# Optimization experiments

Hardware: AMD Instinct MI355X
Metric: run time of the kernel (lower is better)

## Reference

```python
import jax, jax.numpy as jnp
import numpy as np

N, D = 131072, 128   # total nodes, feature size (input_size)
G, L = 512, 448      # num graphs, max padded segment length
EPS = 1e-5


def setup_inputs() -> dict:
    key = jax.random.key(0)
    ks = jax.random.split(key, 8)
    # ragged segment sizes summing exactly to N, each <= L
    rng = np.random.default_rng(0)
    counts = rng.integers(192, 321, size=G)
    diff = N - int(counts.sum())
    idx = rng.integers(0, G, size=abs(diff))
    np.add.at(counts, idx, 1 if diff > 0 else -1)
    assert int(counts.sum()) == N and int(counts.max()) <= L
    batch = jnp.asarray(np.repeat(np.arange(G), counts), dtype=jnp.int32)

    s = 1.0 / np.sqrt(D)
    x = jax.random.normal(ks[0], (N, D), jnp.float32)
    Wk = jax.random.normal(ks[1], (D, D), jnp.float32) * s
    Wq = jax.random.normal(ks[2], (D, D), jnp.float32) * s
    Wv = jax.random.normal(ks[3], (D, D), jnp.float32) * s
    bk = jnp.zeros((D,), jnp.float32)
    bq = jnp.zeros((D,), jnp.float32)
    bv = jnp.zeros((D,), jnp.float32)
    gamma = jnp.ones((D,), jnp.float32)
    beta = jnp.zeros((D,), jnp.float32)
    return {"x": x, "Wk": Wk, "bk": bk, "Wq": Wq, "bq": bq,
            "Wv": Wv, "bv": bv, "gamma": gamma, "beta": beta, "batch": batch}


def reference(x, Wk, bk, Wq, bq, Wv, bv, gamma, beta, batch):
    keys = x @ Wk.T + bk
    query = x @ Wq.T + bq
    values = x @ Wv.T + bv

    counts = jnp.bincount(batch, length=G)                 # [G]
    starts = jnp.cumsum(counts) - counts                   # segment offsets
    pos = jnp.arange(N, dtype=batch.dtype) - starts[batch]  # index within segment

    # scatter ragged nodes into padded [G, L, D] blocks (honors block-diagonal structure)
    kp = jnp.zeros((G, L, D), x.dtype).at[batch, pos].set(keys)
    qp = jnp.zeros((G, L, D), x.dtype).at[batch, pos].set(query)
    vp = jnp.zeros((G, L, D), x.dtype).at[batch, pos].set(values)
    valid = jnp.arange(L)[None, :] < counts[:, None]        # [G, L]

    # NOTE: original computes softmax(K @ Q^T / sqrt(dk)) @ V (keys as rows)
    scale = 1.0 / jnp.sqrt(jnp.asarray(D, x.dtype))
    scores = jnp.einsum('gld,gmd->glm', kp, qp) * scale     # [G, L, L]
    scores = jnp.where(valid[:, None, :], scores, jnp.asarray(-1e9, x.dtype))
    attn = jax.nn.softmax(scores, axis=-1)
    zp = jnp.einsum('glm,gmd->gld', attn, vp)               # [G, L, D]
    z = zp[batch, pos]                                      # back to ragged [N, D]

    h = x + z
    mu = jnp.mean(h, axis=-1, keepdims=True)
    var = jnp.var(h, axis=-1, keepdims=True)
    return (h - mu) / jnp.sqrt(var + EPS) * gamma + beta
```

## Files before the change

### kernel.cpp

```cpp
#include <hip/hip_runtime.h>
#include <hip/hip_bf16.h>

#define N_NODES 131072
#define DIM 128
#define NG 512

typedef __bf16 bf16;
typedef __attribute__((ext_vector_type(8))) __bf16 bf16x8;
typedef __attribute__((ext_vector_type(4))) float f32x4;

#define KSC 0.12753785006196978f

#define WS_STARTS 0
#define WS_WF     8192
#define WS_KB     131072
#define WS_QB     (131072 + 33554432)
#define WS_VTB    (131072 + 2*33554432)

__device__ __forceinline__ void gl_lds16(const void* g, void* l) {
    __builtin_amdgcn_global_load_lds(
        (const __attribute__((address_space(1))) unsigned int*)g,
        (__attribute__((address_space(3))) unsigned int*)l, 16, 0, 0);
}

__global__ void seg_starts_kernel(const int* __restrict__ batch, int* __restrict__ starts) {
    int g = threadIdx.x;
    int lo = 0, hi = N_NODES;
    while (lo < hi) { int mid = (lo + hi) >> 1; if (batch[mid] < g) lo = mid + 1; else hi = mid; }
    starts[g] = lo;
    if (g == 0) starts[NG] = N_NODES;
}

__global__ void wconv_kernel(const float* __restrict__ Wk, const float* __restrict__ Wq,
                             const float* __restrict__ Wv, bf16* __restrict__ Wf) {
    int f = blockIdx.x * 256 + threadIdx.x;
    int lane = f & 63, ks = (f >> 6) & 3, n0 = (f >> 8) & 7, mat = f >> 11;
    const float* src = (mat == 0) ? Wk : ((mat == 1) ? Wq : Wv);
    float sc = (mat == 0) ? KSC : 1.0f;
    int col = n0 * 16 + (lane & 15);
    int koff = ks * 32 + (lane >> 4) * 8;
    const float* p = src + col * DIM + koff;
    bf16* dst = Wf + (size_t)f * 8;
    #pragma unroll
    for (int j = 0; j < 8; j++) dst[j] = (bf16)(p[j] * sc);
}

__global__ __launch_bounds__(256) void qkv_kernel(
        const float* __restrict__ x, const bf16* __restrict__ Wf,
        const float* __restrict__ bk, const float* __restrict__ bq, const float* __restrict__ bv,
        bf16* __restrict__ Kb, bf16* __restrict__ Qb, bf16* __restrict__ Vtb) {
    __shared__ bf16 tile[128 * 136];
    const int tid = threadIdx.x;
    const int w = tid >> 6, lane = tid & 63, q = lane >> 4, i = lane & 15;
    const int r0 = blockIdx.x * 128;

    {
        #pragma unroll
        for (int it = 0; it < 16; it++) {
            int e = tid * 4 + it * 1024;
            int row = e >> 7, col = e & 127;
            float4 u = *(const float4*)(x + (size_t)(r0 + row) * DIM + col);
            bf16 b[4] = {(bf16)u.x, (bf16)u.y, (bf16)u.z, (bf16)u.w};
            *(ushort4*)&tile[row * 136 + col] = *(ushort4*)b;
        }
    }
    __syncthreads();

    bf16x8 af[2][4];
    #pragma unroll
    for (int rg = 0; rg < 2; rg++)
        #pragma unroll
        for (int ks = 0; ks < 4; ks++)
            af[rg][ks] = *(const bf16x8*)&tile[(w * 32 + rg * 16 + i) * 136 + ks * 32 + q * 8];
    __syncthreads();

    for (int mat = 0; mat < 3; mat++) {
        const float* bias = (mat == 0) ? bk : ((mat == 1) ? bq : bv);
        const float bscale = (mat == 0) ? KSC : 1.0f;
        for (int n0 = 0; n0 < 8; n0++) {
            int col = n0 * 16 + i;
            float bias_v = bias[col] * bscale;
            f32x4 acc0 = {0,0,0,0}, acc1 = {0,0,0,0};
            #pragma unroll
            for (int ks = 0; ks < 4; ks++) {
                bf16x8 bw = *(const bf16x8*)(Wf + ((size_t)((mat * 8 + n0) * 4 + ks) * 64 + lane) * 8);
                acc0 = __builtin_amdgcn_mfma_f32_16x16x32_bf16(af[0][ks], bw, acc0, 0, 0, 0);
                acc1 = __builtin_amdgcn_mfma_f32_16x16x32_bf16(af[1][ks], bw, acc1, 0, 0, 0);
            }
            #pragma unroll
            for (int rg = 0; rg < 2; rg++) {
                f32x4 a = rg ? acc1 : acc0;
                #pragma unroll
                for (int r = 0; r < 4; r++) {
                    int rowl = w * 32 + rg * 16 + q * 4 + r;
                    bf16 hv = (bf16)(a[r] + bias_v);
                    if (mat < 2) tile[rowl * 136 + col] = hv;
                    else         tile[col * 136 + rowl] = hv;
                }
            }
        }
        __syncthreads();
        {
            int row = tid >> 1, half = tid & 1;
            const uint4* src = (const uint4*)(tile + row * 136 + half * 64);
            uint4* dst;
            if (mat == 0)      dst = (uint4*)(Kb  + (size_t)(r0 + row) * DIM + half * 64);
            else if (mat == 1) dst = (uint4*)(Qb  + (size_t)(r0 + row) * DIM + half * 64);
            else               dst = (uint4*)(Vtb + (size_t)row * N_NODES + r0 + half * 64);
            #pragma unroll
            for (int j = 0; j < 8; j++) dst[j] = src[j];
        }
        __syncthreads();
    }
}

__global__ __launch_bounds__(256, 2) void attn_kernel(
        const float* __restrict__ x,
        const bf16* __restrict__ Kb, const bf16* __restrict__ Qb, const bf16* __restrict__ Vtb,
        const float* __restrict__ gamma, const float* __restrict__ beta,
        const int* __restrict__ starts, float* __restrict__ out) {
    __shared__ bf16 Qs[2][64 * 128];
    __shared__ bf16 Vts[2][128 * 64];
    __shared__ bf16 Ps[4][32 * 64];

    const int g = blockIdx.y;
    const int seg = starts[g];
    const int c = starts[g + 1] - seg;
    const int l0 = blockIdx.x * 128;
    if (l0 >= c) return;

    const int tid = threadIdx.x;
    const int w = tid >> 6, lane = tid & 63, q = lane >> 4, i = lane & 15;

    const int mstart = seg & ~7;
    const int nch = (seg - mstart + c + 63) >> 6;

    auto stage = [&](int buf, int mb) {
        const int rb = w * 16;
        #pragma unroll
        for (int p = 0; p < 4; p++) {
            int row = rb + p * 4 + (lane >> 4);
            int gr = mb + row; if (gr > N_NODES - 1) gr = N_NODES - 1;
            gl_lds16(Qb + (size_t)gr * DIM + (((lane & 15) ^ (row & 7)) << 3),
                     &Qs[buf][(rb + p * 4) * 128]);
        }
        const int db = w * 32;
        #pragma unroll
        for (int p = 0; p < 4; p++) {
            int d = db + p * 8 + (lane >> 3);
            int mo = mb + (((lane & 7) ^ (d & 7)) << 3);
            if (mo > N_NODES - 8) mo = N_NODES - 8;
            gl_lds16(Vtb + (size_t)d * N_NODES + mo,
                     &Vts[buf][(db + p * 8) * 64]);
        }
    };

    stage(0, mstart);

    bf16x8 afK[2][4];
    #pragma unroll
    for (int rg = 0; rg < 2; rg++) {
        int lrow = l0 + w * 32 + rg * 16 + i;
        if (lrow > c - 1) lrow = c - 1;
        const bf16* krow = Kb + (size_t)(seg + lrow) * DIM;
        #pragma unroll
        for (int ks = 0; ks < 4; ks++)
            afK[rg][ks] = *(const bf16x8*)(krow + ks * 32 + q * 8);
    }

    float li[2][4] = {{0,0,0,0},{0,0,0,0}};
    f32x4 Oc[2][8];
    #pragma unroll
    for (int rg = 0; rg < 2; rg++)
        #pragma unroll
        for (int t = 0; t < 8; t++) Oc[rg][t] = (f32x4){0,0,0,0};

    bf16* Pw = Ps[w];
    const int f7 = i & 7;
    const int mh = (i >> 3);

    for (int mc = 0; mc < nch; mc++) {
        const int cur = mc & 1;
        const int mbase = mstart + (mc << 6);
        __syncthreads();
        if (mc + 1 < nch) stage(cur ^ 1, mbase + 64);

        const bf16* QsB = Qs[cur];
        const bf16* VtB = Vts[cur];

        #pragma unroll
        for (int ti = 0; ti < 4; ti++) {
            f32x4 a0 = {0,0,0,0}, a1 = {0,0,0,0};
            #pragma unroll
            for (int ks = 0; ks < 4; ks++) {
                bf16x8 bq = *(const bf16x8*)&QsB[(ti * 16 + i) * 128 + (((ks * 4 + q) ^ f7) << 3)];
                a0 = __builtin_amdgcn_mfma_f32_16x16x32_bf16(afK[0][ks], bq, a0, 0, 0, 0);
                a1 = __builtin_amdgcn_mfma_f32_16x16x32_bf16(afK[1][ks], bq, a1, 0, 0, 0);
            }
            if (mc == 0 || mc == nch - 1) {
                int mg = mbase + ti * 16 + i;
                if (mg < seg || mg >= seg + c) {
                    a0 = (f32x4){-1.0e30f, -1.0e30f, -1.0e30f, -1.0e30f};
                    a1 = a0;
                }
            }
            int mhi = 2 * ti + mh;
            #pragma unroll
            for (int r = 0; r < 4; r++) {
                int lr = q * 4 + r;
                int sl = ((mhi ^ (lr & 7)) << 3) + f7;
                float p0 = exp2f(a0[r]); li[0][r] += p0;
                Pw[lr * 64 + sl] = (bf16)p0;
                float p1 = exp2f(a1[r]); li[1][r] += p1;
                Pw[(16 + lr) * 64 + sl] = (bf16)p1;
            }
        }

        bf16x8 afP[2][2];
        #pragma unroll
        for (int rg = 0; rg < 2; rg++)
            #pragma unroll
            for (int k2 = 0; k2 < 2; k2++)
                afP[rg][k2] = *(const bf16x8*)&Pw[(rg * 16 + i) * 64 + (((k2 * 4 + q) ^ f7) << 3)];

        #pragma unroll
        for (int dt = 0; dt < 8; dt++) {
            #pragma unroll
            for (int k2 = 0; k2 < 2; k2++) {
                bf16x8 bv = *(const bf16x8*)&VtB[(dt * 16 + i) * 64 + (((k2 * 4 + q) ^ f7) << 3)];
                Oc[0][dt] = __builtin_amdgcn_mfma_f32_16x16x32_bf16(afP[0][k2], bv, Oc[0][dt], 0, 0, 0);
                Oc[1][dt] = __builtin_amdgcn_mfma_f32_16x16x32_bf16(afP[1][k2], bv, Oc[1][dt], 0, 0, 0);
            }
        }
    }

    #pragma unroll
    for (int st = 1; st < 16; st <<= 1)
        #pragma unroll
        for (int rg = 0; rg < 2; rg++)
            #pragma unroll
            for (int r = 0; r < 4; r++)
                li[rg][r] += __shfl_xor(li[rg][r], st);

    float gv[8], bvv[8];
    #pragma unroll
    for (int t = 0; t < 8; t++) { gv[t] = gamma[t * 16 + i]; bvv[t] = beta[t * 16 + i]; }
    #pragma unroll
    for (int rg = 0; rg < 2; rg++)
        for (int r = 0; r < 4; r++) {
            int lg = l0 + w * 32 + rg * 16 + q * 4 + r;
            if (lg >= c) continue;
            size_t node = (size_t)(seg + lg);
            float inv = 1.0f / li[rg][r];
            const float* xr = x + node * DIM;
            float h[8], sum = 0.0f, ss = 0.0f;
            #pragma unroll
            for (int t = 0; t < 8; t++) {
                float hv = xr[t * 16 + i] + Oc[rg][t][r] * inv;
                h[t] = hv;
                sum += hv; ss += hv * hv;
            }
            #pragma unroll
            for (int st = 1; st < 16; st <<= 1) {
                sum += __shfl_xor(sum, st);
                ss  += __shfl_xor(ss, st);
            }
            float mu = sum * (1.0f / 128.0f);
            float var = ss * (1.0f / 128.0f) - mu * mu;
            float rstd = rsqrtf(var + 1e-5f);
            float* op = out + node * DIM;
            #pragma unroll
            for (int t = 0; t < 8; t++)
                op[t * 16 + i] = (h[t] - mu) * rstd * gv[t] + bvv[t];
        }
}

extern "C" void kernel_launch(void* const* d_in, const int* in_sizes, int n_in,
                              void* d_out, int out_size, void* d_ws, size_t ws_size,
                              hipStream_t stream) {
    (void)in_sizes; (void)n_in; (void)out_size; (void)ws_size;
    const float* x     = (const float*)d_in[0];
    const float* Wk    = (const float*)d_in[1];
    const float* bk    = (const float*)d_in[2];
    const float* Wq    = (const float*)d_in[3];
    const float* bq    = (const float*)d_in[4];
    const float* Wv    = (const float*)d_in[5];
    const float* bv    = (const float*)d_in[6];
    const float* gamma = (const float*)d_in[7];
    const float* beta  = (const float*)d_in[8];
    const int*   batch = (const int*)d_in[9];
    float* out = (float*)d_out;

    char* ws = (char*)d_ws;
    int*  starts = (int*)(ws + WS_STARTS);
    bf16* Wf  = (bf16*)(ws + WS_WF);
    bf16* Kb  = (bf16*)(ws + WS_KB);
    bf16* Qb  = (bf16*)(ws + WS_QB);
    bf16* Vtb = (bf16*)(ws + WS_VTB);

    seg_starts_kernel<<<1, 512, 0, stream>>>(batch, starts);
    wconv_kernel<<<24, 256, 0, stream>>>(Wk, Wq, Wv, Wf);
    qkv_kernel<<<1024, 256, 0, stream>>>(x, Wf, bk, bq, bv, Kb, Qb, Vtb);
    attn_kernel<<<dim3(4, NG), 256, 0, stream>>>(x, Kb, Qb, Vtb, gamma, beta, starts, out);
}
```

Measured before the change: 277.3 us.

## Triple-buffer attention chunks at 32 keys, reuse Q LDS for P, raise occupancy

The attention kernel now processes 32-key chunks with a 3-stage LDS ring buffer, using explicit vmcnt waits and raw barriers so loads run two chunks ahead. The separate P scratch buffer is removed and P is written into the consumed Q buffer, which cuts LDS use so launch bounds can rise to 3 blocks per CU. It also adds MFMA priority hints and swaps the grid so graph is on the x dimension. Smaller chunks mean more barriers per key, and the hand-written waitcnt logic relies on exact load counts per stage.

```diff
diff --git a/kernel.cpp b/kernel.cpp
--- a/kernel.cpp
+++ b/kernel.cpp
@@ -114,48 +114,44 @@
     }
 }
 
-__global__ __launch_bounds__(256, 2) void attn_kernel(
+__global__ __launch_bounds__(256, 3) void attn_kernel(
         const float* __restrict__ x,
         const bf16* __restrict__ Kb, const bf16* __restrict__ Qb, const bf16* __restrict__ Vtb,
         const float* __restrict__ gamma, const float* __restrict__ beta,
         const int* __restrict__ starts, float* __restrict__ out) {
-    __shared__ bf16 Qs[2][64 * 128];
-    __shared__ bf16 Vts[2][128 * 64];
-    __shared__ bf16 Ps[4][32 * 64];
-
-    const int g = blockIdx.y;
+    __shared__ bf16 Qs[3][32 * 128];
+    __shared__ bf16 Vts[3][128 * 32];
+
+    const int g = blockIdx.x;
     const int seg = starts[g];
     const int c = starts[g + 1] - seg;
-    const int l0 = blockIdx.x * 128;
+    const int l0 = blockIdx.y * 128;
     if (l0 >= c) return;
 
     const int tid = threadIdx.x;
     const int w = tid >> 6, lane = tid & 63, q = lane >> 4, i = lane & 15;
 
     const int mstart = seg & ~7;
-    const int nch = (seg - mstart + c + 63) >> 6;
+    const int nch = (seg - mstart + c + 31) >> 5;
 
     auto stage = [&](int buf, int mb) {
-        const int rb = w * 16;
-        #pragma unroll
-        for (int p = 0; p < 4; p++) {
-            int row = rb + p * 4 + (lane >> 4);
+        #pragma unroll
+        for (int p = 0; p < 2; p++) {
+            int row = w * 8 + p * 4 + (lane >> 4);
             int gr = mb + row; if (gr > N_NODES - 1) gr = N_NODES - 1;
             gl_lds16(Qb + (size_t)gr * DIM + (((lane & 15) ^ (row & 7)) << 3),
-                     &Qs[buf][(rb + p * 4) * 128]);
-        }
-        const int db = w * 32;
-        #pragma unroll
-        for (int p = 0; p < 4; p++) {
-            int d = db + p * 8 + (lane >> 3);
-            int mo = mb + (((lane & 7) ^ (d & 7)) << 3);
+                     &Qs[buf][(w * 8 + p * 4) * 128]);
+        }
+        #pragma unroll
+        for (int p = 0; p < 2; p++) {
+            int d = w * 32 + p * 16 + (lane >> 2);
+            int tvd = ((lane >> 2) ^ (lane >> 4)) & 3;
+            int mo = mb + (((lane & 3) ^ tvd) << 3);
             if (mo > N_NODES - 8) mo = N_NODES - 8;
             gl_lds16(Vtb + (size_t)d * N_NODES + mo,
-                     &Vts[buf][(db + p * 8) * 64]);
+                     &Vts[buf][(w * 32 + p * 16) * 32]);
         }
     };
-
-    stage(0, mstart);
 
     bf16x8 afK[2][4];
     #pragma unroll
@@ -168,6 +164,9 @@
             afK[rg][ks] = *(const bf16x8*)(krow + ks * 32 + q * 8);
     }
 
+    stage(0, mstart);
+    if (nch > 1) stage(1, mstart + 32);
+
     float li[2][4] = {{0,0,0,0},{0,0,0,0}};
     f32x4 Oc[2][8];
     #pragma unroll
@@ -175,21 +174,26 @@
         #pragma unroll
         for (int t = 0; t < 8; t++) Oc[rg][t] = (f32x4){0,0,0,0};
 
-    bf16* Pw = Ps[w];
     const int f7 = i & 7;
-    const int mh = (i >> 3);
+    const int tvi = (i ^ (i >> 2)) & 3;
 
     for (int mc = 0; mc < nch; mc++) {
-        const int cur = mc & 1;
-        const int mbase = mstart + (mc << 6);
-        __syncthreads();
-        if (mc + 1 < nch) stage(cur ^ 1, mbase + 64);
+        const int cur = mc % 3;
+        const int mbase = mstart + (mc << 5);
+        if (mc + 1 < nch) asm volatile("s_waitcnt vmcnt(4)" ::: "memory");
+        else              asm volatile("s_waitcnt vmcnt(0)" ::: "memory");
+        __builtin_amdgcn_s_barrier();
+        __builtin_amdgcn_sched_barrier(0);
+        if (mc + 2 < nch) stage((mc + 2) % 3, mbase + 64);
 
         const bf16* QsB = Qs[cur];
         const bf16* VtB = Vts[cur];
-
-        #pragma unroll
-        for (int ti = 0; ti < 4; ti++) {
+        bf16* Pw = &Qs[cur][w * 1024];
+
+        f32x4 s[2][2];
+        __builtin_amdgcn_s_setprio(1);
+        #pragma unroll
+        for (int ti = 0; ti < 2; ti++) {
             f32x4 a0 = {0,0,0,0}, a1 = {0,0,0,0};
             #pragma unroll
             for (int ks = 0; ks < 4; ks++) {
@@ -197,41 +201,59 @@
                 a0 = __builtin_amdgcn_mfma_f32_16x16x32_bf16(afK[0][ks], bq, a0, 0, 0, 0);
                 a1 = __builtin_amdgcn_mfma_f32_16x16x32_bf16(afK[1][ks], bq, a1, 0, 0, 0);
             }
-            if (mc == 0 || mc == nch - 1) {
+            s[0][ti] = a0; s[1][ti] = a1;
+        }
+        __builtin_amdgcn_s_setprio(0);
+        if (mc == 0 || mc == nch - 1) {
+            #pragma unroll
+            for (int ti = 0; ti < 2; ti++) {
                 int mg = mbase + ti * 16 + i;
-                if (mg < seg || mg >= seg + c) {
-                    a0 = (f32x4){-1.0e30f, -1.0e30f, -1.0e30f, -1.0e30f};
-                    a1 = a0;
+                bool valid = (mg >= seg) && (mg < seg + c);
+                if (!valid) {
+                    s[0][ti] = (f32x4){-1.0e30f, -1.0e30f, -1.0e30f, -1.0e30f};
+                    s[1][ti] = s[0][ti];
                 }
             }
-            int mhi = 2 * ti + mh;
-            #pragma unroll
-            for (int r = 0; r < 4; r++) {
-                int lr = q * 4 + r;
-                int sl = ((mhi ^ (lr & 7)) << 3) + f7;
-                float p0 = exp2f(a0[r]); li[0][r] += p0;
-                Pw[lr * 64 + sl] = (bf16)p0;
-                float p1 = exp2f(a1[r]); li[1][r] += p1;
-                Pw[(16 + lr) * 64 + sl] = (bf16)p1;
-            }
-        }
-
-        bf16x8 afP[2][2];
+        }
         #pragma unroll
         for (int rg = 0; rg < 2; rg++)
             #pragma unroll
-            for (int k2 = 0; k2 < 2; k2++)
-                afP[rg][k2] = *(const bf16x8*)&Pw[(rg * 16 + i) * 64 + (((k2 * 4 + q) ^ f7) << 3)];
-
+            for (int ti = 0; ti < 2; ti++)
+                #pragma unroll
+                for (int r = 0; r < 4; r++) {
+                    float pv = exp2f(s[rg][ti][r]);
+                    li[rg][r] += pv;
+                    s[rg][ti][r] = pv;
+                }
+
+        asm volatile("s_waitcnt lgkmcnt(0)" ::: "memory");
+        __builtin_amdgcn_s_barrier();
+        __builtin_amdgcn_sched_barrier(0);
+
+        #pragma unroll
+        for (int rg = 0; rg < 2; rg++)
+            #pragma unroll
+            for (int ti = 0; ti < 2; ti++)
+                #pragma unroll
+                for (int r = 0; r < 4; r++) {
+                    int rowl = rg * 16 + q * 4 + r;
+                    int slot = (ti * 2 + (i >> 3)) ^ (q ^ r);
+                    Pw[rowl * 32 + slot * 8 + f7] = (bf16)s[rg][ti][r];
+                }
+
+        bf16x8 afP[2];
+        #pragma unroll
+        for (int rg = 0; rg < 2; rg++)
+            afP[rg] = *(const bf16x8*)&Pw[(rg * 16 + i) * 32 + ((q ^ tvi) << 3)];
+
+        __builtin_amdgcn_s_setprio(1);
         #pragma unroll
         for (int dt = 0; dt < 8; dt++) {
-            #pragma unroll
-            for (int k2 = 0; k2 < 2; k2++) {
-                bf16x8 bv = *(const bf16x8*)&VtB[(dt * 16 + i) * 64 + (((k2 * 4 + q) ^ f7) << 3)];
-                Oc[0][dt] = __builtin_amdgcn_mfma_f32_16x16x32_bf16(afP[0][k2], bv, Oc[0][dt], 0, 0, 0);
-                Oc[1][dt] = __builtin_amdgcn_mfma_f32_16x16x32_bf16(afP[1][k2], bv, Oc[1][dt], 0, 0, 0);
-            }
-        }
+            bf16x8 bv = *(const bf16x8*)&VtB[(dt * 16 + i) * 32 + ((q ^ tvi) << 3)];
+            Oc[0][dt] = __builtin_amdgcn_mfma_f32_16x16x32_bf16(afP[0], bv, Oc[0][dt], 0, 0, 0);
+            Oc[1][dt] = __builtin_amdgcn_mfma_f32_16x16x32_bf16(afP[1], bv, Oc[1][dt], 0, 0, 0);
+        }
+        __builtin_amdgcn_s_setprio(0);
     }
 
     #pragma unroll
@@ -301,5 +323,5 @@
     seg_starts_kernel<<<1, 512, 0, stream>>>(batch, starts);
     wconv_kernel<<<24, 256, 0, stream>>>(Wk, Wq, Wv, Wf);
     qkv_kernel<<<1024, 256, 0, stream>>>(x, Wf, bk, bq, bv, Kb, Qb, Vtb);
-    attn_kernel<<<dim3(4, NG), 256, 0, stream>>>(x, Kb, Qb, Vtb, gamma, beta, starts, out);
-}
+    attn_kernel<<<dim3(NG, 4), 256, 0, stream>>>(x, Kb, Qb, Vtb, gamma, beta, starts, out);
+}
```

Measured after the change: 251.0 us. 1.1x faster.
